# Kernel optimization log

Hardware: AMD Instinct MI355X
Metric: run time of the kernel (lower is better)

Reference implementation:

```python
import jax, jax.numpy as jnp
import numpy as np

B, N, C = 8, 4096, 3
IN_DIM = 2
HID = 512
NL = 256          # num_latents
DEPTH = 6
H, DH = 8, 64     # heads, dim_head (cross and latent)
INNER = H * DH
LAT = 32          # latent (bottleneck) dim
NF, MAXF = 12, 4  # NeRF num_freq, max_freq_log2
FF = 4 * HID
SCALE = DH ** -0.5
NERF_DIM = 2 * NF * IN_DIM  # 48


def layer_norm(x, g, b, eps=1e-5):
    m = jnp.mean(x, axis=-1, keepdims=True)
    v = jnp.mean((x - m) ** 2, axis=-1, keepdims=True)
    return (x - m) * jax.lax.rsqrt(v + eps) * g + b


def nerf_encode(pos):
    # log-sampled frequency bands: 2^linspace(0, MAXF, NF)
    freqs = 2.0 ** jnp.linspace(0.0, float(MAXF), NF)
    ang = pos[..., None] * freqs            # [B,N,IN_DIM,NF]
    enc = jnp.concatenate([jnp.sin(ang), jnp.cos(ang)], axis=-1)  # [B,N,IN_DIM,2NF]
    return enc.reshape(*pos.shape[:-1], NERF_DIM)


def mha(q, k, v):
    # q:[B,Nq,INNER] k,v:[B,Nk,INNER] -> [B,Nq,INNER]
    def split(t):
        b, n, _ = t.shape
        return t.reshape(b, n, H, DH).transpose(0, 2, 1, 3)  # [B,H,n,DH]
    qh, kh, vh = split(q), split(k), split(v)
    sim = jnp.einsum('bhid,bhjd->bhij', qh, kh) * SCALE
    attn = jax.nn.softmax(sim, axis=-1)
    o = jnp.einsum('bhij,bhjd->bhid', attn, vh)
    return o.transpose(0, 2, 1, 3).reshape(q.shape[0], q.shape[1], INNER)


def setup_inputs():
    key = jax.random.key(0)
    ks = iter(jax.random.split(key, 64))
    def w(*shape):
        return jax.random.normal(next(ks), shape, jnp.float32) * 0.02
    inp = {}
    inp['x'] = jax.random.normal(next(ks), (B, N, C), jnp.float32)
    inp['pos'] = jax.random.uniform(next(ks), (B, N, IN_DIM), jnp.float32)
    # input embeddings
    inp['W_pos'] = w(NERF_DIM, HID); inp['b_pos'] = jnp.zeros((HID,), jnp.float32)
    inp['W_in'] = w(C, HID); inp['b_in'] = jnp.zeros((HID,), jnp.float32)
    inp['latents'] = w(NL, HID)
    # cross-attention (PreNormCross: norm on q, k, v)
    for n in ('lnq', 'lnk', 'lnv'):
        inp[n + '_g'] = jnp.ones((HID,), jnp.float32)
        inp[n + '_b'] = jnp.zeros((HID,), jnp.float32)
    inp['cWq'] = w(HID, INNER); inp['cWk'] = w(HID, INNER); inp['cWv'] = w(HID, INNER)
    inp['cWo'] = w(INNER, HID); inp['c_bo'] = jnp.zeros((HID,), jnp.float32)
    # self-attention + FFN stacks
    inp['ln1_g'] = jnp.ones((DEPTH, HID), jnp.float32); inp['ln1_b'] = jnp.zeros((DEPTH, HID), jnp.float32)
    inp['sWq'] = w(DEPTH, HID, INNER); inp['sWkv'] = w(DEPTH, HID, 2 * INNER)
    inp['sWo'] = w(DEPTH, INNER, HID); inp['s_bo'] = jnp.zeros((DEPTH, HID), jnp.float32)
    inp['ln2_g'] = jnp.ones((DEPTH, HID), jnp.float32); inp['ln2_b'] = jnp.zeros((DEPTH, HID), jnp.float32)
    inp['fW1'] = w(DEPTH, HID, FF); inp['f_b1'] = jnp.zeros((DEPTH, FF), jnp.float32)
    inp['fW2'] = w(DEPTH, FF, HID); inp['f_b2'] = jnp.zeros((DEPTH, HID), jnp.float32)
    # final norm + gaussian bottleneck projection (mean, logvar)
    inp['lnf_g'] = jnp.ones((HID,), jnp.float32); inp['lnf_b'] = jnp.zeros((HID,), jnp.float32)
    inp['Wb'] = w(HID, 2 * LAT); inp['bb'] = jnp.zeros((2 * LAT,), jnp.float32)
    return inp


def reference(x, pos, W_pos, b_pos, W_in, b_in, latents,
              lnq_g, lnq_b, lnk_g, lnk_b, lnv_g, lnv_b,
              cWq, cWk, cWv, cWo, c_bo,
              ln1_g, ln1_b, sWq, sWkv, sWo, s_bo,
              ln2_g, ln2_b, fW1, f_b1, fW2, f_b2,
              lnf_g, lnf_b, Wb, bb):
    # positional embedding (FourierPositionalEmbedding with relu)
    kin = jax.nn.relu(nerf_encode(pos) @ W_pos + b_pos)   # [B,N,HID]
    vin = x @ W_in + b_in                                 # [B,N,HID]
    vin = vin + kin                                       # include_pos_in_value
    lat = jnp.broadcast_to(latents, (B, NL, HID))
    # cross-attention block (PreNormCross + residual)
    qn = layer_norm(lat, lnq_g, lnq_b)
    kn = layer_norm(kin, lnk_g, lnk_b)
    vn = layer_norm(vin, lnv_g, lnv_b)
    o = mha(qn @ cWq, kn @ cWk, vn @ cWv) @ cWo + c_bo
    lat = lat + o
    # latent self-attention + FFN blocks
    for i in range(DEPTH):
        h1 = layer_norm(lat, ln1_g[i], ln1_b[i])
        q = h1 @ sWq[i]
        k, v = jnp.split(h1 @ sWkv[i], 2, axis=-1)
        lat = lat + (mha(q, k, v) @ sWo[i] + s_bo[i])
        h2 = layer_norm(lat, ln2_g[i], ln2_b[i])
        lat = lat + (jax.nn.gelu(h2 @ fW1[i] + f_b1[i]) @ fW2[i] + f_b2[i])
    # bottleneck projection -> (mean | logvar)
    out = layer_norm(lat, lnf_g, lnf_b) @ Wb + bb         # [B,NL,2*LAT]
    return out
```

## Files before the change

### kernel.cpp

```cpp
#include <hip/hip_runtime.h>
#include <hip/hip_bf16.h>

#define DEV __device__ __forceinline__

typedef __attribute__((ext_vector_type(8))) short short8;
typedef __attribute__((ext_vector_type(4))) float floatx4;

DEV short f2bf(float f) {
  unsigned u = __float_as_uint(f);
  u += 0x7fffu + ((u >> 16) & 1u);
  return (short)(u >> 16);
}
DEV float bf2f(short s) {
  return __uint_as_float(((unsigned)(unsigned short)s) << 16);
}
DEV float wred(float v) {
#pragma unroll
  for (int m = 1; m < 64; m <<= 1) v += __shfl_xor(v, m);
  return v;
}
DEV floatx4 mfma16(short8 a, short8 b, floatx4 c) {
  return __builtin_amdgcn_mfma_f32_16x16x32_bf16(a, b, c, 0, 0, 0);
}
DEV void gload16(void* lds, const void* g) {
  __builtin_amdgcn_global_load_lds(
      (const __attribute__((address_space(1))) unsigned int*)g,
      (__attribute__((address_space(3))) unsigned int*)lds, 16, 0, 0);
}

struct MatDesc { const float* src; int K; int N; int kp; int off; };
struct MatTable { MatDesc m[36]; };

__global__ __launch_bounds__(256) void wtrans_kernel(MatTable T, short* __restrict__ dst) {
  int mi = blockIdx.y;
  MatDesc d = T.m[mi];
  int tilesx = d.N >> 5, tilesy = d.kp >> 5;
  int tb = blockIdx.x;
  if (tb >= tilesx * tilesy) return;
  int ty = tb / tilesx, tx = tb % tilesx;
  __shared__ float tile[32][33];
  int tid = threadIdx.x;
#pragma unroll
  for (int i = 0; i < 4; ++i) {
    int e = tid + i * 256, lr = e >> 5, lc = e & 31;
    int kk = ty * 32 + lr;
    tile[lr][lc] = (kk < d.K) ? d.src[(size_t)kk * d.N + tx * 32 + lc] : 0.f;
  }
  __syncthreads();
#pragma unroll
  for (int i = 0; i < 4; ++i) {
    int e = tid + i * 256, lr = e >> 5, lc = e & 31;
    dst[(size_t)d.off + (size_t)(tx * 32 + lr) * d.kp + ty * 32 + lc] = f2bf(tile[lc][lr]);
  }
}

__global__ __launch_bounds__(256) void enc_kernel(const float* __restrict__ pos,
                                                  short* __restrict__ enc) {
  int idx = blockIdx.x * 256 + threadIdx.x;
  int row = idx >> 3, oct = idx & 7;
  float p0 = pos[row * 2], p1 = pos[row * 2 + 1];
  short8 o;
#pragma unroll
  for (int j = 0; j < 8; ++j) {
    int k = oct * 8 + j;
    float val = 0.f;
    if (k < 48) {
      int dd = k / 24, rem = k % 24;
      int trig = rem / 12, f = rem % 12;
      float ang = (dd ? p1 : p0) * exp2f((4.0f / 11.0f) * (float)f);
      val = trig ? __cosf(ang) : __sinf(ang);
    }
    o[j] = f2bf(val);
  }
  *(short8*)&enc[(size_t)row * 64 + oct * 8] = o;
}

__global__ __launch_bounds__(512) void embed2_kernel(
    const short* __restrict__ enc, const short* __restrict__ Wt,
    const float* __restrict__ b_pos, const float* __restrict__ W_in,
    const float* __restrict__ b_in, const float* __restrict__ x,
    const float* __restrict__ lnk_g, const float* __restrict__ lnk_b,
    const float* __restrict__ lnv_g, const float* __restrict__ lnv_b,
    short* __restrict__ knvn) {
  __shared__ short Wl[512 * 64];
  __shared__ short El[128 * 64];
  int tid = threadIdx.x;
  int lane = tid & 63, wv = tid >> 6;
  int c = lane & 15, g = lane >> 4;
  int blk = blockIdx.x * 128;
#pragma unroll
  for (int gi = 0; gi < 8; ++gi) {
    int grp = wv * 8 + gi;
    int row = grp * 8 + (lane >> 3), kc = lane & 7;
    gload16(&Wl[grp * 512], &Wt[(size_t)row * 64 + ((kc ^ (row & 7)) * 8)]);
  }
#pragma unroll
  for (int gi = 0; gi < 2; ++gi) {
    int grp = wv * 2 + gi;
    int row = grp * 8 + (lane >> 3), kc = lane & 7;
    gload16(&El[grp * 512], &enc[(size_t)(blk + row) * 64 + ((kc ^ (row & 7)) * 8)]);
  }
  __syncthreads();

  floatx4 acc[32];
  floatx4 zf = {0.f, 0.f, 0.f, 0.f};
#pragma unroll
  for (int nf = 0; nf < 32; ++nf) acc[nf] = zf;
  short8 af[2];
#pragma unroll
  for (int ks = 0; ks < 2; ++ks)
    af[ks] = *(const short8*)&El[(wv * 16 + c) * 64 + ((ks * 4 + g) ^ (c & 7)) * 8];
#pragma unroll
  for (int nf = 0; nf < 32; ++nf) {
#pragma unroll
    for (int ks = 0; ks < 2; ++ks) {
      short8 bf8 = *(const short8*)&Wl[(nf * 16 + c) * 64 + ((ks * 4 + g) ^ (c & 7)) * 8];
      acc[nf] = mfma16(af[ks], bf8, acc[nf]);
    }
  }

  int rowbase = blk + wv * 16 + g * 4;
  float x0[4], x1[4], x2[4];
  float s1[4], q1[4], s2[4], q2[4];
#pragma unroll
  for (int r = 0; r < 4; ++r) {
    x0[r] = x[(size_t)(rowbase + r) * 3];
    x1[r] = x[(size_t)(rowbase + r) * 3 + 1];
    x2[r] = x[(size_t)(rowbase + r) * 3 + 2];
    s1[r] = 0; q1[r] = 0; s2[r] = 0; q2[r] = 0;
  }
#pragma unroll
  for (int nf = 0; nf < 32; ++nf) {
    int col = nf * 16 + c;
    float bp = b_pos[col];
    float w0 = W_in[col], w1 = W_in[512 + col], w2 = W_in[1024 + col], bi = b_in[col];
#pragma unroll
    for (int r = 0; r < 4; ++r) {
      float kk = fmaxf(acc[nf][r] + bp, 0.f);
      float vv = kk + x0[r] * w0 + x1[r] * w1 + x2[r] * w2 + bi;
      acc[nf][r] = kk;
      s1[r] += kk; q1[r] += kk * kk; s2[r] += vv; q2[r] += vv * vv;
    }
  }
  float m1[4], r1[4], m2[4], r2[4];
#pragma unroll
  for (int r = 0; r < 4; ++r) {
#pragma unroll
    for (int msk = 1; msk < 16; msk <<= 1) {
      s1[r] += __shfl_xor(s1[r], msk); q1[r] += __shfl_xor(q1[r], msk);
      s2[r] += __shfl_xor(s2[r], msk); q2[r] += __shfl_xor(q2[r], msk);
    }
    m1[r] = s1[r] * (1.f / 512.f);
    r1[r] = rsqrtf(q1[r] * (1.f / 512.f) - m1[r] * m1[r] + 1e-5f);
    m2[r] = s2[r] * (1.f / 512.f);
    r2[r] = rsqrtf(q2[r] * (1.f / 512.f) - m2[r] * m2[r] + 1e-5f);
  }
#pragma unroll
  for (int nf = 0; nf < 32; ++nf) {
    int col = nf * 16 + c;
    float w0 = W_in[col], w1 = W_in[512 + col], w2 = W_in[1024 + col], bi = b_in[col];
    float gk = lnk_g[col], bk = lnk_b[col], gv = lnv_g[col], bv = lnv_b[col];
#pragma unroll
    for (int r = 0; r < 4; ++r) {
      float kk = acc[nf][r];
      float vv = kk + x0[r] * w0 + x1[r] * w1 + x2[r] * w2 + bi;
      size_t ridx = (size_t)(rowbase + r) * 1024;
      knvn[ridx + col] = f2bf((kk - m1[r]) * r1[r] * gk + bk);
      knvn[ridx + 512 + col] = f2bf((vv - m2[r]) * r2[r] * gv + bv);
    }
  }
}

__global__ __launch_bounds__(256) void ln_kernel(
    const float* __restrict__ in, const float* __restrict__ g,
    const float* __restrict__ b, short* __restrict__ out, int M) {
  int row = blockIdx.x * 4 + (threadIdx.x >> 6);
  if (row >= M) return;
  int lane = threadIdx.x & 63;
  float v[8]; float s = 0, q = 0;
#pragma unroll
  for (int j = 0; j < 8; ++j) {
    v[j] = in[(size_t)row * 512 + lane + 64 * j];
    s += v[j]; q += v[j] * v[j];
  }
  s = wred(s); q = wred(q);
  float m = s * (1.f / 512.f);
  float rs = rsqrtf(q * (1.f / 512.f) - m * m + 1e-5f);
#pragma unroll
  for (int j = 0; j < 8; ++j) {
    int cc = lane + 64 * j;
    out[(size_t)row * 512 + cc] = f2bf((v[j] - m) * rs * g[cc] + b[cc]);
  }
}

__global__ void bcast_kernel(const float* __restrict__ latents, float* __restrict__ lat) {
  int i = blockIdx.x * 256 + threadIdx.x;
  lat[i] = latents[i & 131071];
}

template <int EPI>
DEV void epi_store(void* outp, size_t idx, float xv) {
  if (EPI == 0) {
    ((short*)outp)[idx] = f2bf(xv);
  } else if (EPI == 1) {
    float t = 0.7978845608f * (xv + 0.044715f * xv * xv * xv);
    ((short*)outp)[idx] = f2bf(0.5f * xv * (1.f + tanhf(t)));
  } else if (EPI == 2) {
    ((float*)outp)[idx] += xv;
  } else {
    ((float*)outp)[idx] = xv;
  }
}

template <int EPI>
__global__ __launch_bounds__(256) void gemm_kernel(
    const short* __restrict__ A, const short* __restrict__ Wt,
    const float* __restrict__ bias, void* __restrict__ outp,
    int M, int N, int K, int lda, int ldo) {
  __shared__ short Alds[128 * 64];
  __shared__ short Blds[128 * 64];
  int tid = threadIdx.x;
  int brow = blockIdx.y * 128, bcol = blockIdx.x * 128;
  int lane = tid & 63, wvid = tid >> 6;
  int wr = wvid >> 1, wc = wvid & 1;
  int g = lane >> 4, c = lane & 15;
  floatx4 zf = {0.f, 0.f, 0.f, 0.f};
  floatx4 acc[4][4];
#pragma unroll
  for (int i = 0; i < 4; ++i)
#pragma unroll
    for (int j = 0; j < 4; ++j) acc[i][j] = zf;

  int srow = (lane >> 3), skc = lane & 7;
  for (int k0 = 0; k0 < K; k0 += 64) {
#pragma unroll
    for (int gi = 0; gi < 4; ++gi) {
      int grp = wvid * 4 + gi;
      int row = grp * 8 + srow;
      int sw = ((skc ^ (row & 7)) * 8);
      gload16(&Alds[grp * 512], &A[(size_t)(brow + row) * lda + k0 + sw]);
      gload16(&Blds[grp * 512], &Wt[(size_t)(bcol + row) * K + k0 + sw]);
    }
    __syncthreads();
#pragma unroll
    for (int ks = 0; ks < 2; ++ks) {
      int slot = ((ks * 4 + g) ^ (c & 7)) * 8;
      short8 af[4], bf8[4];
#pragma unroll
      for (int mf = 0; mf < 4; ++mf)
        af[mf] = *(const short8*)&Alds[(wr * 64 + mf * 16 + c) * 64 + slot];
#pragma unroll
      for (int nf = 0; nf < 4; ++nf)
        bf8[nf] = *(const short8*)&Blds[(wc * 64 + nf * 16 + c) * 64 + slot];
#pragma unroll
      for (int mf = 0; mf < 4; ++mf)
#pragma unroll
        for (int nf = 0; nf < 4; ++nf)
          acc[mf][nf] = mfma16(af[mf], bf8[nf], acc[mf][nf]);
    }
    __syncthreads();
  }

#pragma unroll
  for (int mf = 0; mf < 4; ++mf) {
#pragma unroll
    for (int nf = 0; nf < 4; ++nf) {
      int col = bcol + wc * 64 + nf * 16 + c;
      float bv = bias ? bias[col] : 0.f;
      int row0 = brow + wr * 64 + mf * 16 + g * 4;
#pragma unroll
      for (int r = 0; r < 4; ++r)
        epi_store<EPI>(outp, (size_t)(row0 + r) * ldo + col, acc[mf][nf][r] + bv);
    }
  }
}

template <int EPI>
__global__ __launch_bounds__(256) void gemm64_kernel(
    const short* __restrict__ A, const short* __restrict__ Wt,
    const float* __restrict__ bias, void* __restrict__ outp,
    int M, int N, int K, int lda, int ldo) {
  __shared__ short Alds[64 * 64];
  __shared__ short Blds[64 * 64];
  int tid = threadIdx.x;
  int brow = blockIdx.y * 64, bcol = blockIdx.x * 64;
  int lane = tid & 63, wvid = tid >> 6;
  int wr = wvid >> 1, wc = wvid & 1;
  int g = lane >> 4, c = lane & 15;
  floatx4 zf = {0.f, 0.f, 0.f, 0.f};
  floatx4 acc[2][2];
#pragma unroll
  for (int i = 0; i < 2; ++i)
#pragma unroll
    for (int j = 0; j < 2; ++j) acc[i][j] = zf;

  int srow = (lane >> 3), skc = lane & 7;
  for (int k0 = 0; k0 < K; k0 += 64) {
#pragma unroll
    for (int gi = 0; gi < 2; ++gi) {
      int grp = wvid * 2 + gi;
      int row = grp * 8 + srow;
      int sw = ((skc ^ (row & 7)) * 8);
      gload16(&Alds[grp * 512], &A[(size_t)(brow + row) * lda + k0 + sw]);
      gload16(&Blds[grp * 512], &Wt[(size_t)(bcol + row) * K + k0 + sw]);
    }
    __syncthreads();
#pragma unroll
    for (int ks = 0; ks < 2; ++ks) {
      int slot = ((ks * 4 + g) ^ (c & 7)) * 8;
      short8 af[2], bf8[2];
#pragma unroll
      for (int mf = 0; mf < 2; ++mf)
        af[mf] = *(const short8*)&Alds[(wr * 32 + mf * 16 + c) * 64 + slot];
#pragma unroll
      for (int nf = 0; nf < 2; ++nf)
        bf8[nf] = *(const short8*)&Blds[(wc * 32 + nf * 16 + c) * 64 + slot];
#pragma unroll
      for (int mf = 0; mf < 2; ++mf)
#pragma unroll
        for (int nf = 0; nf < 2; ++nf)
          acc[mf][nf] = mfma16(af[mf], bf8[nf], acc[mf][nf]);
    }
    __syncthreads();
  }

#pragma unroll
  for (int mf = 0; mf < 2; ++mf) {
#pragma unroll
    for (int nf = 0; nf < 2; ++nf) {
      int col = bcol + wc * 32 + nf * 16 + c;
      float bv = bias ? bias[col] : 0.f;
      int row0 = brow + wr * 32 + mf * 16 + g * 4;
#pragma unroll
      for (int r = 0; r < 4; ++r)
        epi_store<EPI>(outp, (size_t)(row0 + r) * ldo + col, acc[mf][nf][r] + bv);
    }
  }
}

__global__ __launch_bounds__(256) void flashsp_kernel(
    const short* __restrict__ q, const short* __restrict__ k,
    const short* __restrict__ v, float* __restrict__ po,
    float* __restrict__ pm, float* __restrict__ pl,
    int qrs, int qbrows, long kvbstride, int kvrstride,
    int seglen, int lognseg) {
  __shared__ short Qs[64 * 64];
  __shared__ short Ks[64 * 64];
  __shared__ short Vt[64 * 72];
  __shared__ short Ps[64 * 72];
  int tid = threadIdx.x;
  int bz = blockIdx.z;
  int b = bz >> lognseg, seg = bz & ((1 << lognseg) - 1);
  int h = blockIdx.y, qt = blockIdx.x;
  int lane = tid & 63, wv = tid >> 6;
  int g = lane >> 4, c = lane & 15;
  int srow = lane >> 3, skc = lane & 7;

#pragma unroll
  for (int gi = 0; gi < 2; ++gi) {
    int grp = wv * 2 + gi;
    int row = grp * 8 + srow;
    int sw = ((skc ^ (row & 7)) * 8);
    gload16(&Qs[grp * 512],
            &q[((size_t)(b * qbrows) + qt * 64 + row) * qrs + h * 64 + sw]);
  }

  float m_[4], l_[4];
  floatx4 zf = {0.f, 0.f, 0.f, 0.f};
  floatx4 o_[4];
#pragma unroll
  for (int r = 0; r < 4; ++r) { m_[r] = -3.0e38f; l_[r] = 0.f; }
#pragma unroll
  for (int f = 0; f < 4; ++f) o_[f] = zf;

  int tbeg = seg * seglen, tend = tbeg + seglen;
  for (int t0 = tbeg; t0 < tend; t0 += 64) {
#pragma unroll
    for (int gi = 0; gi < 2; ++gi) {
      int grp = wv * 2 + gi;
      int row = grp * 8 + srow;
      int sw = ((skc ^ (row & 7)) * 8);
      gload16(&Ks[grp * 512],
              &k[(size_t)b * kvbstride + (size_t)(t0 + row) * kvrstride + h * 64 + sw]);
    }
#pragma unroll
    for (int it = 0; it < 2; ++it) {
      int ch = tid + it * 256;
      int j = ch >> 3, f0 = (ch & 7) * 8, mm = ch & 7, tg = j >> 3;
      short8 tv = *(const short8*)&v[(size_t)b * kvbstride + (size_t)(t0 + j) * kvrstride + h * 64 + f0];
#pragma unroll
      for (int jj = 0; jj < 8; ++jj)
        Vt[(f0 + jj) * 72 + ((tg ^ mm) * 8) + (j & 7)] = tv[jj];
    }
    __syncthreads();

    floatx4 s[4];
#pragma unroll
    for (int f = 0; f < 4; ++f) s[f] = zf;
#pragma unroll
    for (int ks = 0; ks < 2; ++ks) {
      int slot = ((ks * 4 + g) ^ (c & 7)) * 8;
      short8 a = *(const short8*)&Qs[(wv * 16 + c) * 64 + slot];
#pragma unroll
      for (int f = 0; f < 4; ++f) {
        short8 b8 = *(const short8*)&Ks[(f * 16 + c) * 64 + slot];
        s[f] = mfma16(a, b8, s[f]);
      }
    }
#pragma unroll
    for (int f = 0; f < 4; ++f)
#pragma unroll
      for (int r = 0; r < 4; ++r) s[f][r] *= 0.125f;

    float nm[4], sf[4], rs[4];
#pragma unroll
    for (int r = 0; r < 4; ++r) {
      float t = fmaxf(fmaxf(s[0][r], s[1][r]), fmaxf(s[2][r], s[3][r]));
#pragma unroll
      for (int msk = 1; msk < 16; msk <<= 1) t = fmaxf(t, __shfl_xor(t, msk));
      nm[r] = fmaxf(m_[r], t);
      sf[r] = __expf(m_[r] - nm[r]);
      rs[r] = 0.f;
    }
#pragma unroll
    for (int f = 0; f < 4; ++f)
#pragma unroll
      for (int r = 0; r < 4; ++r) {
        float p = __expf(s[f][r] - nm[r]);
        s[f][r] = p; rs[r] += p;
      }
#pragma unroll
    for (int r = 0; r < 4; ++r) {
#pragma unroll
      for (int msk = 1; msk < 16; msk <<= 1) rs[r] += __shfl_xor(rs[r], msk);
      l_[r] = l_[r] * sf[r] + rs[r];
      m_[r] = nm[r];
    }
#pragma unroll
    for (int f = 0; f < 4; ++f)
#pragma unroll
      for (int r = 0; r < 4; ++r) o_[f][r] *= sf[r];
#pragma unroll
    for (int f = 0; f < 4; ++f)
#pragma unroll
      for (int r = 0; r < 4; ++r)
        Ps[(wv * 16 + g * 4 + r) * 72 + f * 16 + c] = f2bf(s[f][r]);
    __syncthreads();
#pragma unroll
    for (int ks = 0; ks < 2; ++ks) {
      short8 pa = *(const short8*)&Ps[(wv * 16 + c) * 72 + ks * 32 + g * 8];
#pragma unroll
      for (int f = 0; f < 4; ++f) {
        int mm = (2 * f + (c >> 3)) & 7;
        short8 vb = *(const short8*)&Vt[(f * 16 + c) * 72 + ((ks * 4 + g) ^ mm) * 8];
        o_[f] = mfma16(pa, vb, o_[f]);
      }
    }
    __syncthreads();
  }

#pragma unroll
  for (int f = 0; f < 4; ++f)
#pragma unroll
    for (int r = 0; r < 4; ++r) {
      int row = qt * 64 + wv * 16 + g * 4 + r;
      size_t grow = (size_t)seg * 2048 + b * 256 + row;
      po[grow * 512 + h * 64 + f * 16 + c] = o_[f][r];
      if (f == 0 && c == 0) {
        pm[grow * 8 + h] = m_[r];
        pl[grow * 8 + h] = l_[r];
      }
    }
}

template <int NSEG>
__global__ __launch_bounds__(256) void fcomb_kernel(
    const float* __restrict__ po, const float* __restrict__ pm,
    const float* __restrict__ pl, short* __restrict__ out) {
  int idx = blockIdx.x * 256 + threadIdx.x;
  int grow = idx >> 9, col = idx & 511, h = col >> 6;
  float ms[NSEG];
  float M = -3.0e38f;
#pragma unroll
  for (int s = 0; s < NSEG; ++s) {
    ms[s] = pm[((size_t)s * 2048 + grow) * 8 + h];
    M = fmaxf(M, ms[s]);
  }
  float L = 0.f, acc = 0.f;
#pragma unroll
  for (int s = 0; s < NSEG; ++s) {
    float w = __expf(ms[s] - M);
    L += w * pl[((size_t)s * 2048 + grow) * 8 + h];
    acc += w * po[((size_t)s * 2048 + grow) * 512 + col];
  }
  out[idx] = f2bf(acc / L);
}

extern "C" void kernel_launch(void* const* d_in, const int* in_sizes, int n_in,
                              void* d_out, int out_size, void* d_ws, size_t ws_size,
                              hipStream_t stream) {
  const float* x       = (const float*)d_in[0];
  const float* pos     = (const float*)d_in[1];
  const float* W_pos   = (const float*)d_in[2];
  const float* b_pos   = (const float*)d_in[3];
  const float* W_in    = (const float*)d_in[4];
  const float* b_in    = (const float*)d_in[5];
  const float* latents = (const float*)d_in[6];
  const float* lnq_g   = (const float*)d_in[7];
  const float* lnq_b   = (const float*)d_in[8];
  const float* lnk_g   = (const float*)d_in[9];
  const float* lnk_b   = (const float*)d_in[10];
  const float* lnv_g   = (const float*)d_in[11];
  const float* lnv_b   = (const float*)d_in[12];
  const float* cWq     = (const float*)d_in[13];
  const float* cWk     = (const float*)d_in[14];
  const float* cWv     = (const float*)d_in[15];
  const float* cWo     = (const float*)d_in[16];
  const float* c_bo    = (const float*)d_in[17];
  const float* ln1_g   = (const float*)d_in[18];
  const float* ln1_b   = (const float*)d_in[19];
  const float* sWq     = (const float*)d_in[20];
  const float* sWkv    = (const float*)d_in[21];
  const float* sWo     = (const float*)d_in[22];
  const float* s_bo    = (const float*)d_in[23];
  const float* ln2_g   = (const float*)d_in[24];
  const float* ln2_b   = (const float*)d_in[25];
  const float* fW1     = (const float*)d_in[26];
  const float* f_b1    = (const float*)d_in[27];
  const float* fW2     = (const float*)d_in[28];
  const float* f_b2    = (const float*)d_in[29];
  const float* lnf_g   = (const float*)d_in[30];
  const float* lnf_b   = (const float*)d_in[31];
  const float* Wb      = (const float*)d_in[32];
  const float* bbv     = (const float*)d_in[33];
  float* outp = (float*)d_out;

  size_t W = 0;
  size_t o_cWq = W; W += 512 * 512;
  size_t o_cWk = W; W += 512 * 512;
  size_t o_cWv = W; W += 512 * 512;
  size_t o_cWo = W; W += 512 * 512;
  size_t o_Wb  = W; W += 64 * 512;
  size_t o_Wpos = W; W += 512 * 64;
  size_t o_sQKV[6], o_sWo[6], o_fW1[6], o_fW2[6];
  for (int i = 0; i < 6; ++i) {
    o_sQKV[i] = W; W += 1536 * 512;
    o_sWo[i]  = W; W += 512 * 512;
    o_fW1[i]  = W; W += 2048 * 512;
    o_fW2[i]  = W; W += 512 * 2048;
  }
  MatTable T;
  int nm = 0;
  auto add = [&](const float* s, int K, int N, int kp, size_t off) {
    T.m[nm].src = s; T.m[nm].K = K; T.m[nm].N = N; T.m[nm].kp = kp;
    T.m[nm].off = (int)off; ++nm;
  };
  add(cWq, 512, 512, 512, o_cWq); add(cWk, 512, 512, 512, o_cWk);
  add(cWv, 512, 512, 512, o_cWv); add(cWo, 512, 512, 512, o_cWo);
  add(Wb, 512, 64, 512, o_Wb);
  add(W_pos, 48, 512, 64, o_Wpos);
  for (int i = 0; i < 6; ++i) {
    add(sWq  + (size_t)i * 512 * 512,  512, 512,  512, o_sQKV[i]);
    add(sWkv + (size_t)i * 512 * 1024, 512, 1024, 512, o_sQKV[i] + 512 * 512);
    add(sWo  + (size_t)i * 512 * 512,  512, 512,  512, o_sWo[i]);
    add(fW1  + (size_t)i * 512 * 2048, 512, 2048, 512, o_fW1[i]);
    add(fW2  + (size_t)i * 2048 * 512, 2048, 512, 2048, o_fW2[i]);
  }

  char* p = (char*)d_ws;
  auto carve = [&](size_t bytes) {
    char* r = p; p += (bytes + 255) & ~(size_t)255; return r;
  };
  short* wtb   = (short*)carve(W * 2);
  short* enc   = (short*)carve((size_t)32768 * 64 * 2);
  short* knvn  = (short*)carve((size_t)32768 * 1024 * 2);
  short* kvc   = (short*)carve((size_t)32768 * 1024 * 2);
  short* latn0 = (short*)carve(262144);
  short* qc    = (short*)carve(262144);
  float* lat   = (float*)carve(4194304);
  float* pm    = (float*)carve(1048576);
  float* pl    = (float*)carve(1048576);
  short* attno = enc;
  float* po    = (float*)knvn;
  short* h     = (short*)((char*)knvn + 36 * 1048576);
  short* qkv   = (short*)((char*)knvn + 40 * 1048576);
  short* ffh   = (short*)((char*)knvn + 48 * 1048576);

  wtrans_kernel<<<dim3(1024, 36), 256, 0, stream>>>(T, wtb);
  enc_kernel<<<1024, 256, 0, stream>>>(pos, enc);
  embed2_kernel<<<256, 512, 0, stream>>>(enc, wtb + o_Wpos, b_pos, W_in, b_in, x,
                                         lnk_g, lnk_b, lnv_g, lnv_b, knvn);
  bcast_kernel<<<4096, 256, 0, stream>>>(latents, lat);
  ln_kernel<<<64, 256, 0, stream>>>(latents, lnq_g, lnq_b, latn0, 256);
  gemm64_kernel<0><<<dim3(8, 4), 256, 0, stream>>>(latn0, wtb + o_cWq, nullptr, qc, 256, 512, 512, 512, 512);
  gemm_kernel<0><<<dim3(4, 256), 256, 0, stream>>>(knvn, wtb + o_cWk, nullptr, kvc, 32768, 512, 512, 1024, 1024);
  gemm_kernel<0><<<dim3(4, 256), 256, 0, stream>>>(knvn + 512, wtb + o_cWv, nullptr, kvc + 512, 32768, 512, 512, 1024, 1024);
  flashsp_kernel<<<dim3(4, 8, 64), 256, 0, stream>>>(qc, kvc, kvc + 512, po, pm, pl,
                                                     512, 0, (long)4096 * 1024, 1024, 512, 3);
  fcomb_kernel<8><<<4096, 256, 0, stream>>>(po, pm, pl, attno);
  gemm64_kernel<2><<<dim3(8, 32), 256, 0, stream>>>(attno, wtb + o_cWo, c_bo, lat, 2048, 512, 512, 512, 512);

  for (int i = 0; i < 6; ++i) {
    ln_kernel<<<512, 256, 0, stream>>>(lat, ln1_g + i * 512, ln1_b + i * 512, h, 2048);
    gemm64_kernel<0><<<dim3(24, 32), 256, 0, stream>>>(h, wtb + o_sQKV[i], nullptr, qkv, 2048, 1536, 512, 512, 1536);
    flashsp_kernel<<<dim3(4, 8, 16), 256, 0, stream>>>(qkv, qkv + 512, qkv + 1024, po, pm, pl,
                                                       1536, 256, (long)256 * 1536, 1536, 128, 1);
    fcomb_kernel<2><<<4096, 256, 0, stream>>>(po, pm, pl, attno);
    gemm64_kernel<2><<<dim3(8, 32), 256, 0, stream>>>(attno, wtb + o_sWo[i], s_bo + i * 512, lat, 2048, 512, 512, 512, 512);
    ln_kernel<<<512, 256, 0, stream>>>(lat, ln2_g + i * 512, ln2_b + i * 512, h, 2048);
    gemm64_kernel<1><<<dim3(32, 32), 256, 0, stream>>>(h, wtb + o_fW1[i], f_b1 + i * 2048, ffh, 2048, 2048, 512, 512, 2048);
    gemm64_kernel<2><<<dim3(8, 32), 256, 0, stream>>>(ffh, wtb + o_fW2[i], f_b2 + i * 512, lat, 2048, 512, 2048, 2048, 512);
  }
  ln_kernel<<<512, 256, 0, stream>>>(lat, lnf_g, lnf_b, h, 2048);
  gemm64_kernel<3><<<dim3(1, 32), 256, 0, stream>>>(h, wtb + o_Wb, bbv, outp, 2048, 64, 512, 512, 64);
}
```

Measured before the change: 798.9 us.

## Fold attention scale into Wq, stage embed params in LDS, XCD-swizzle GEMM tiles

The softmax scale is folded into the Q projection weights during the bf16 weight transpose, which removes the per-score multiply in the flash attention kernel. The embedding kernel now stages the bias, W_in and layer-norm parameters in shared memory instead of re-reading them from global memory in its epilogue loops. The 128x128 GEMM remaps block IDs so consecutive tiles spread across the eight XCDs. The FFN up-projection switches from the 64-tile GEMM to the 128-tile GEMM. Scaling Q before the bf16 rounding changes rounding slightly, and the extra LDS in the embed kernel may reduce its occupancy.

```diff
diff --git a/kernel.cpp b/kernel.cpp
--- a/kernel.cpp
+++ b/kernel.cpp
@@ -28,7 +28,7 @@
       (__attribute__((address_space(3))) unsigned int*)lds, 16, 0, 0);
 }
 
-struct MatDesc { const float* src; int K; int N; int kp; int off; };
+struct MatDesc { const float* src; int K; int N; int kp; int off; float scale; };
 struct MatTable { MatDesc m[36]; };
 
 __global__ __launch_bounds__(256) void wtrans_kernel(MatTable T, short* __restrict__ dst) {
@@ -50,7 +50,8 @@
 #pragma unroll
   for (int i = 0; i < 4; ++i) {
     int e = tid + i * 256, lr = e >> 5, lc = e & 31;
-    dst[(size_t)d.off + (size_t)(tx * 32 + lr) * d.kp + ty * 32 + lc] = f2bf(tile[lc][lr]);
+    dst[(size_t)d.off + (size_t)(tx * 32 + lr) * d.kp + ty * 32 + lc] =
+        f2bf(tile[lc][lr] * d.scale);
   }
 }
 
@@ -84,6 +85,7 @@
     short* __restrict__ knvn) {
   __shared__ short Wl[512 * 64];
   __shared__ short El[128 * 64];
+  __shared__ float Pf[9 * 512];
   int tid = threadIdx.x;
   int lane = tid & 63, wv = tid >> 6;
   int c = lane & 15, g = lane >> 4;
@@ -100,6 +102,15 @@
     int row = grp * 8 + (lane >> 3), kc = lane & 7;
     gload16(&El[grp * 512], &enc[(size_t)(blk + row) * 64 + ((kc ^ (row & 7)) * 8)]);
   }
+  Pf[tid]        = b_pos[tid];
+  Pf[512 + tid]  = W_in[tid];
+  Pf[1024 + tid] = W_in[512 + tid];
+  Pf[1536 + tid] = W_in[1024 + tid];
+  Pf[2048 + tid] = b_in[tid];
+  Pf[2560 + tid] = lnk_g[tid];
+  Pf[3072 + tid] = lnk_b[tid];
+  Pf[3584 + tid] = lnv_g[tid];
+  Pf[4096 + tid] = lnv_b[tid];
   __syncthreads();
 
   floatx4 acc[32];
@@ -132,8 +143,8 @@
 #pragma unroll
   for (int nf = 0; nf < 32; ++nf) {
     int col = nf * 16 + c;
-    float bp = b_pos[col];
-    float w0 = W_in[col], w1 = W_in[512 + col], w2 = W_in[1024 + col], bi = b_in[col];
+    float bp = Pf[col];
+    float w0 = Pf[512 + col], w1 = Pf[1024 + col], w2 = Pf[1536 + col], bi = Pf[2048 + col];
 #pragma unroll
     for (int r = 0; r < 4; ++r) {
       float kk = fmaxf(acc[nf][r] + bp, 0.f);
@@ -158,8 +169,9 @@
 #pragma unroll
   for (int nf = 0; nf < 32; ++nf) {
     int col = nf * 16 + c;
-    float w0 = W_in[col], w1 = W_in[512 + col], w2 = W_in[1024 + col], bi = b_in[col];
-    float gk = lnk_g[col], bk = lnk_b[col], gv = lnv_g[col], bv = lnv_b[col];
+    float w0 = Pf[512 + col], w1 = Pf[1024 + col], w2 = Pf[1536 + col], bi = Pf[2048 + col];
+    float gk = Pf[2560 + col], bk = Pf[3072 + col];
+    float gv = Pf[3584 + col], bv = Pf[4096 + col];
 #pragma unroll
     for (int r = 0; r < 4; ++r) {
       float kk = acc[nf][r];
@@ -220,7 +232,11 @@
   __shared__ short Alds[128 * 64];
   __shared__ short Blds[128 * 64];
   int tid = threadIdx.x;
-  int brow = blockIdx.y * 128, bcol = blockIdx.x * 128;
+  int nwg = gridDim.x * gridDim.y;
+  int id = blockIdx.y * gridDim.x + blockIdx.x;
+  int cpx = nwg >> 3;
+  id = (id & 7) * cpx + (id >> 3);
+  int brow = (id / gridDim.x) * 128, bcol = (id % gridDim.x) * 128;
   int lane = tid & 63, wvid = tid >> 6;
   int wr = wvid >> 1, wc = wvid & 1;
   int g = lane >> 4, c = lane & 15;
@@ -407,10 +423,6 @@
         s[f] = mfma16(a, b8, s[f]);
       }
     }
-#pragma unroll
-    for (int f = 0; f < 4; ++f)
-#pragma unroll
-      for (int r = 0; r < 4; ++r) s[f][r] *= 0.125f;
 
     float nm[4], sf[4], rs[4];
 #pragma unroll
@@ -551,20 +563,21 @@
   }
   MatTable T;
   int nm = 0;
-  auto add = [&](const float* s, int K, int N, int kp, size_t off) {
+  auto add = [&](const float* s, int K, int N, int kp, size_t off, float sc) {
     T.m[nm].src = s; T.m[nm].K = K; T.m[nm].N = N; T.m[nm].kp = kp;
-    T.m[nm].off = (int)off; ++nm;
+    T.m[nm].off = (int)off; T.m[nm].scale = sc; ++nm;
   };
-  add(cWq, 512, 512, 512, o_cWq); add(cWk, 512, 512, 512, o_cWk);
-  add(cWv, 512, 512, 512, o_cWv); add(cWo, 512, 512, 512, o_cWo);
-  add(Wb, 512, 64, 512, o_Wb);
-  add(W_pos, 48, 512, 64, o_Wpos);
+  const float SC = 0.125f;
+  add(cWq, 512, 512, 512, o_cWq, SC); add(cWk, 512, 512, 512, o_cWk, 1.f);
+  add(cWv, 512, 512, 512, o_cWv, 1.f); add(cWo, 512, 512, 512, o_cWo, 1.f);
+  add(Wb, 512, 64, 512, o_Wb, 1.f);
+  add(W_pos, 48, 512, 64, o_Wpos, 1.f);
   for (int i = 0; i < 6; ++i) {
-    add(sWq  + (size_t)i * 512 * 512,  512, 512,  512, o_sQKV[i]);
-    add(sWkv + (size_t)i * 512 * 1024, 512, 1024, 512, o_sQKV[i] + 512 * 512);
-    add(sWo  + (size_t)i * 512 * 512,  512, 512,  512, o_sWo[i]);
-    add(fW1  + (size_t)i * 512 * 2048, 512, 2048, 512, o_fW1[i]);
-    add(fW2  + (size_t)i * 2048 * 512, 2048, 512, 2048, o_fW2[i]);
+    add(sWq  + (size_t)i * 512 * 512,  512, 512,  512, o_sQKV[i], SC);
+    add(sWkv + (size_t)i * 512 * 1024, 512, 1024, 512, o_sQKV[i] + 512 * 512, 1.f);
+    add(sWo  + (size_t)i * 512 * 512,  512, 512,  512, o_sWo[i], 1.f);
+    add(fW1  + (size_t)i * 512 * 2048, 512, 2048, 512, o_fW1[i], 1.f);
+    add(fW2  + (size_t)i * 2048 * 512, 2048, 512, 2048, o_fW2[i], 1.f);
   }
 
   char* p = (char*)d_ws;
@@ -608,7 +621,7 @@
     fcomb_kernel<2><<<4096, 256, 0, stream>>>(po, pm, pl, attno);
     gemm64_kernel<2><<<dim3(8, 32), 256, 0, stream>>>(attno, wtb + o_sWo[i], s_bo + i * 512, lat, 2048, 512, 512, 512, 512);
     ln_kernel<<<512, 256, 0, stream>>>(lat, ln2_g + i * 512, ln2_b + i * 512, h, 2048);
-    gemm64_kernel<1><<<dim3(32, 32), 256, 0, stream>>>(h, wtb + o_fW1[i], f_b1 + i * 2048, ffh, 2048, 2048, 512, 512, 2048);
+    gemm_kernel<1><<<dim3(16, 16), 256, 0, stream>>>(h, wtb + o_fW1[i], f_b1 + i * 2048, ffh, 2048, 2048, 512, 512, 2048);
     gemm64_kernel<2><<<dim3(8, 32), 256, 0, stream>>>(ffh, wtb + o_fW2[i], f_b2 + i * 512, lat, 2048, 512, 2048, 2048, 512);
   }
   ln_kernel<<<512, 256, 0, stream>>>(lat, lnf_g, lnf_b, h, 2048);
```

Result: slower. 818.4 us (+2.4%).
